# Kernel optimization log

Hardware: AMD Instinct MI355X
Metric: run time of the kernel (lower is better)

The kernel has to match this reference:

```python
import jax, jax.numpy as jnp
import numpy as np

NUM_HEADS = 16
HEAD_DIM = 64


def setup_inputs() -> dict:
    key = jax.random.key(0)
    k1, k2, k3 = jax.random.split(key, 3)
    B, S, D = 2, 2048, 1024
    scale = 1.0 / np.sqrt(D)
    return {
        "x": jax.random.normal(k1, (B, S, D), dtype=jnp.float32),
        "W_qkv": jax.random.normal(k2, (D, 3 * D), dtype=jnp.float32) * scale,
        "b_qkv": jnp.zeros((3 * D,), dtype=jnp.float32),
        "W_o": jax.random.normal(k3, (D, D), dtype=jnp.float32) * scale,
        "b_o": jnp.zeros((D,), dtype=jnp.float32),
    }


def reference(x, W_qkv, b_qkv, W_o, b_o):
    B, S, D = x.shape
    H, Hd = NUM_HEADS, HEAD_DIM
    qkv = x @ W_qkv + b_qkv                      # [B, S, 3D]
    qkv = qkv.reshape(B, S, H, 3 * Hd).transpose(0, 2, 1, 3)  # [B, H, S, 3Hd]
    q, k, v = jnp.split(qkv, 3, axis=-1)         # each [B, H, S, Hd]
    # negative squared Euclidean distance: -(|q|^2 - 2 q.k + |k|^2)
    q_sq = jnp.sum(q * q, axis=-1)[..., :, None]   # [B, H, S, 1]
    k_sq = jnp.sum(k * k, axis=-1)[..., None, :]   # [B, H, 1, S]
    qk = jnp.einsum("bhsd,bhtd->bhst", q, k)       # [B, H, S, S]
    logits = -(q_sq - 2.0 * qk + k_sq)
    attn = jax.nn.softmax(logits, axis=-1)
    vals = jnp.einsum("bhst,bhtd->bhsd", attn, v)  # [B, H, S, Hd]
    vals = vals.transpose(0, 2, 1, 3).reshape(B, S, D)
    return vals @ W_o + b_o
```

## Files before the change

kernel.cpp:

```cpp
#include <hip/hip_runtime.h>
#include <hip/hip_bf16.h>

#define NUM_B   2
#define SEQ     2048
#define DMODEL  1024
#define NH      16
#define HD      64
#define M_TOT   (NUM_B * SEQ)
#define N_QKV   (3 * DMODEL)
#define LOG2E   1.4426950408889634f
#define EXP_BIAS 96.0f

typedef __attribute__((ext_vector_type(8))) short short8v;
typedef __attribute__((ext_vector_type(4))) float float4v;
typedef unsigned short ushort_t;

__device__ __forceinline__ ushort_t f2bf(float x) {
    unsigned u = __builtin_bit_cast(unsigned, x);
    u = u + 0x7FFFu + ((u >> 16) & 1u);
    return (ushort_t)(u >> 16);
}
__device__ __forceinline__ float bf2f(ushort_t h) {
    unsigned u = ((unsigned)h) << 16;
    return __builtin_bit_cast(float, u);
}
__device__ __forceinline__ void gll16(const void* g, void* l) {
    __builtin_amdgcn_global_load_lds(
        (const __attribute__((address_space(1))) unsigned int*)g,
        (__attribute__((address_space(3))) unsigned int*)l, 16, 0, 0);
}
__device__ __forceinline__ int sw4(int r) { return (r & 3) ^ ((r >> 2) & 3); }

__global__ __launch_bounds__(256) void prep_kernel(
    const float* __restrict__ Wq, const float* __restrict__ Wo,
    const float* __restrict__ Xf,
    ushort_t* __restrict__ WqT_hi, ushort_t* __restrict__ WqT_lo,
    ushort_t* __restrict__ WoT,
    ushort_t* __restrict__ Xhi, ushort_t* __restrict__ Xlo)
{
    const int bid = blockIdx.x;
    const int t = threadIdx.x;

    if (bid >= 1024) {
        size_t base = (size_t)(bid - 1024) * 4096 + t * 16;
        float xs[16];
        *(float4v*)&xs[0]  = *(const float4v*)(Xf + base);
        *(float4v*)&xs[4]  = *(const float4v*)(Xf + base + 4);
        *(float4v*)&xs[8]  = *(const float4v*)(Xf + base + 8);
        *(float4v*)&xs[12] = *(const float4v*)(Xf + base + 12);
        short8v h0, h1, l0, l1;
        #pragma unroll
        for (int e = 0; e < 8; e++) {
            ushort_t a = f2bf(xs[e]), b = f2bf(xs[8 + e]);
            h0[e] = (short)a; h1[e] = (short)b;
            l0[e] = (short)f2bf(xs[e] - bf2f(a));
            l1[e] = (short)f2bf(xs[8 + e] - bf2f(b));
        }
        *(short8v*)(Xhi + base) = h0; *(short8v*)(Xhi + base + 8) = h1;
        *(short8v*)(Xlo + base) = l0; *(short8v*)(Xlo + base + 8) = l1;
        return;
    }

    __shared__ float Tf[64][65];
    const float* src; ushort_t *dhi, *dlo; int N, k0, n0;
    if (bid < 768) {
        int kt = bid / 48, nt = bid % 48;
        src = Wq; N = N_QKV; dhi = WqT_hi; dlo = WqT_lo;
        k0 = kt * 64; n0 = nt * 64;
    } else {
        int tid = bid - 768;
        int kt = tid >> 4, nt = tid & 15;
        src = Wo; N = DMODEL; dhi = WoT; dlo = nullptr;
        k0 = kt * 64; n0 = nt * 64;
    }
    {
        int r = t >> 2, c0 = (t & 3) * 16;
        const float* srow = src + (size_t)(k0 + r) * N + n0 + c0;
        #pragma unroll
        for (int u = 0; u < 4; u++) {
            float4v f = *(const float4v*)(srow + 4 * u);
            #pragma unroll
            for (int e = 0; e < 4; e++) Tf[r][c0 + 4 * u + e] = f[e];
        }
    }
    __syncthreads();
    {
        int nl = t >> 2, kc = (t & 3) * 16;
        short8v h0, h1, l0, l1;
        #pragma unroll
        for (int e = 0; e < 8; e++) {
            float x0 = Tf[kc + e][nl];
            float x1 = Tf[kc + 8 + e][nl];
            ushort_t a = f2bf(x0), b = f2bf(x1);
            h0[e] = (short)a; h1[e] = (short)b;
            l0[e] = (short)f2bf(x0 - bf2f(a));
            l1[e] = (short)f2bf(x1 - bf2f(b));
        }
        ushort_t* o = dhi + (size_t)(n0 + nl) * 1024 + k0 + kc;
        *(short8v*)o = h0; *(short8v*)(o + 8) = h1;
        if (dlo) {
            ushort_t* o2 = dlo + (size_t)(n0 + nl) * 1024 + k0 + kc;
            *(short8v*)o2 = l0; *(short8v*)(o2 + 8) = l1;
        }
    }
}

template<bool PRE>
__global__ __launch_bounds__(256) void qkv_mfma_kernel(
    const float* __restrict__ X,
    const ushort_t* __restrict__ Xhi, const ushort_t* __restrict__ Xlo,
    const ushort_t* __restrict__ WqT_hi, const ushort_t* __restrict__ WqT_lo,
    const float* __restrict__ bias,
    ushort_t* __restrict__ Qhi, ushort_t* __restrict__ Qlo,
    ushort_t* __restrict__ Khi, ushort_t* __restrict__ Klo,
    ushort_t* __restrict__ Vout,
    float* __restrict__ Qsq, float* __restrict__ Ksq)
{
    __shared__ ushort_t AS2[2 * 128 * 32];
    __shared__ ushort_t BS [2 * 128 * 32];
    const int LO = 128 * 32;
    const int t = threadIdx.x;
    const int w = t >> 6, lane = t & 63;
    const int quad = (t >> 4) & 3, ln = t & 15;
    const int wr = w >> 1, wc = w & 1;
    const int m0 = blockIdx.y * 128, n0 = blockIdx.x * 128;
    const int g = blockIdx.x * 2 + wc;
    const int h = g / 3, part = g % 3;

    const ushort_t* gA[2]; ushort_t* lA[2];
    const float* aptr = nullptr;
    ushort_t *ast_hi0, *ast_hi1, *ast_lo0, *ast_lo1;
    size_t xlo_off = 0;
    if constexpr (PRE) {
        #pragma unroll
        for (int i = 0; i < 2; i++) {
            int c = 256 * i + 64 * w + lane;
            int r = c >> 2, kbp = c & 3;
            gA[i] = Xhi + (size_t)(m0 + r) * 1024 + 8 * (kbp ^ sw4(r));
            lA[i] = &AS2[(256 * i + 64 * w) * 8];
        }
        xlo_off = (size_t)(Xlo - Xhi);
    } else {
        const int arow = t >> 1, akh = t & 1;
        aptr = X + (size_t)(m0 + arow) * DMODEL + 16 * akh;
        const int asw = sw4(arow);
        ast_hi0 = &AS2[arow * 32 + (((2 * akh) ^ asw) << 3)];
        ast_hi1 = &AS2[arow * 32 + (((2 * akh + 1) ^ asw) << 3)];
        ast_lo0 = &AS2[LO + arow * 32 + (((2 * akh) ^ asw) << 3)];
        ast_lo1 = &AS2[LO + arow * 32 + (((2 * akh + 1) ^ asw) << 3)];
    }

    const ushort_t* gB[2]; ushort_t* lB[2];
    #pragma unroll
    for (int i = 0; i < 2; i++) {
        int c = 256 * i + 64 * w + lane;
        int n = c >> 2, kbp = c & 3;
        gB[i] = WqT_hi + (size_t)(n0 + n) * 1024 + 8 * (kbp ^ sw4(n));
        lB[i] = &BS[(256 * i + 64 * w) * 8];
    }
    const size_t lo_goff = (size_t)(WqT_lo - WqT_hi);

    int aoff[4], boff[4];
    #pragma unroll
    for (int i = 0; i < 4; i++) {
        int m_l = 64 * wr + 16 * i + ln;
        aoff[i] = m_l * 32 + ((quad ^ sw4(m_l)) << 3);
        int n_l = 64 * wc + 16 * i + ln;
        boff[i] = n_l * 32 + ((quad ^ sw4(n_l)) << 3);
    }

    float4v acc[4][4];
    #pragma unroll
    for (int i = 0; i < 4; i++)
        #pragma unroll
        for (int j = 0; j < 4; j++) acc[i][j] = (float4v){0.f, 0.f, 0.f, 0.f};

    for (int k0 = 0; k0 < DMODEL; k0 += 32) {
        __syncthreads();
        #pragma unroll
        for (int i = 0; i < 2; i++) {
            gll16(gB[i] + k0, lB[i]);
            gll16(gB[i] + k0 + lo_goff, lB[i] + LO);
        }
        if constexpr (PRE) {
            #pragma unroll
            for (int i = 0; i < 2; i++) {
                gll16(gA[i] + k0, lA[i]);
                gll16(gA[i] + k0 + xlo_off, lA[i] + LO);
            }
        } else {
            float xs[16];
            *(float4v*)&xs[0]  = *(const float4v*)(aptr + k0);
            *(float4v*)&xs[4]  = *(const float4v*)(aptr + k0 + 4);
            *(float4v*)&xs[8]  = *(const float4v*)(aptr + k0 + 8);
            *(float4v*)&xs[12] = *(const float4v*)(aptr + k0 + 12);
            short8v h0, h1, l0, l1;
            #pragma unroll
            for (int e = 0; e < 8; e++) {
                ushort_t a = f2bf(xs[e]), b = f2bf(xs[8 + e]);
                h0[e] = (short)a; h1[e] = (short)b;
                l0[e] = (short)f2bf(xs[e] - bf2f(a));
                l1[e] = (short)f2bf(xs[8 + e] - bf2f(b));
            }
            *(short8v*)ast_hi0 = h0; *(short8v*)ast_hi1 = h1;
            *(short8v*)ast_lo0 = l0; *(short8v*)ast_lo1 = l1;
        }
        __syncthreads();

        short8v ah[4], al[4], bh[4], bl[4];
        #pragma unroll
        for (int i = 0; i < 4; i++) {
            ah[i] = *(short8v*)&AS2[aoff[i]];
            al[i] = *(short8v*)&AS2[LO + aoff[i]];
            bh[i] = *(short8v*)&BS[boff[i]];
            bl[i] = *(short8v*)&BS[LO + boff[i]];
        }
        if (part != 2) {
            #pragma unroll
            for (int mt = 0; mt < 4; mt++)
                #pragma unroll
                for (int nt = 0; nt < 4; nt++) {
                    acc[mt][nt] = __builtin_amdgcn_mfma_f32_16x16x32_bf16(ah[mt], bh[nt], acc[mt][nt], 0, 0, 0);
                    acc[mt][nt] = __builtin_amdgcn_mfma_f32_16x16x32_bf16(ah[mt], bl[nt], acc[mt][nt], 0, 0, 0);
                    acc[mt][nt] = __builtin_amdgcn_mfma_f32_16x16x32_bf16(al[mt], bh[nt], acc[mt][nt], 0, 0, 0);
                }
        } else {
            #pragma unroll
            for (int mt = 0; mt < 4; mt++)
                #pragma unroll
                for (int nt = 0; nt < 4; nt++)
                    acc[mt][nt] = __builtin_amdgcn_mfma_f32_16x16x32_bf16(ah[mt], bh[nt], acc[mt][nt], 0, 0, 0);
        }
    }

    float bvv[4];
    #pragma unroll
    for (int nt = 0; nt < 4; nt++) bvv[nt] = bias[64 * g + 16 * nt + ln];

    #pragma unroll
    for (int mt = 0; mt < 4; mt++) {
        #pragma unroll
        for (int r = 0; r < 4; r++) {
            int m = m0 + 64 * wr + 16 * mt + 4 * quad + r;
            int bb = m >> 11, s = m & (SEQ - 1);
            size_t hsrow = (size_t)(bb * NH + h) * SEQ + s;
            size_t rowbase = hsrow * HD;
            float vv[4];
            #pragma unroll
            for (int nt = 0; nt < 4; nt++) vv[nt] = acc[mt][nt][r] + bvv[nt];
            if (part == 0) {
                float sq = 0.f;
                #pragma unroll
                for (int nt = 0; nt < 4; nt++) {
                    float v = vv[nt];
                    sq += v * v;
                    float v2 = v * (2.0f * LOG2E);
                    ushort_t hb = f2bf(v2);
                    Qhi[rowbase + 16 * nt + ln] = hb;
                    Qlo[rowbase + 16 * nt + ln] = f2bf(v2 - bf2f(hb));
                }
                sq += __shfl_xor(sq, 1); sq += __shfl_xor(sq, 2);
                sq += __shfl_xor(sq, 4); sq += __shfl_xor(sq, 8);
                if (ln == 0) Qsq[hsrow] = sq * LOG2E - EXP_BIAS;
            } else if (part == 1) {
                float sq = 0.f;
                #pragma unroll
                for (int nt = 0; nt < 4; nt++) {
                    float v = vv[nt];
                    sq += v * v;
                    ushort_t hb = f2bf(v);
                    Khi[rowbase + 16 * nt + ln] = hb;
                    Klo[rowbase + 16 * nt + ln] = f2bf(v - bf2f(hb));
                }
                sq += __shfl_xor(sq, 1); sq += __shfl_xor(sq, 2);
                sq += __shfl_xor(sq, 4); sq += __shfl_xor(sq, 8);
                if (ln == 0) Ksq[hsrow] = sq * LOG2E;
            } else {
                if constexpr (PRE) {
                    #pragma unroll
                    for (int nt = 0; nt < 4; nt++)
                        Vout[((size_t)(bb * NH + h) * 64 + 16 * nt + ln) * SEQ + s] = f2bf(vv[nt]);
                } else {
                    #pragma unroll
                    for (int nt = 0; nt < 4; nt++)
                        Vout[rowbase + 16 * nt + ln] = f2bf(vv[nt]);
                }
            }
        }
    }
}

template<bool PRE>
__global__ __launch_bounds__(256) void attn_mfma_kernel(
    const ushort_t* __restrict__ Qhi, const ushort_t* __restrict__ Qlo,
    const ushort_t* __restrict__ Khi, const ushort_t* __restrict__ Klo,
    const ushort_t* __restrict__ Vsrc,
    const float* __restrict__ Qsq, const float* __restrict__ Ksq,
    ushort_t* __restrict__ vals)
{
    __shared__ ushort_t KS[2 * 64 * 64];
    __shared__ ushort_t VtS [64 * 64];
    __shared__ ushort_t PsS [128 * 72];
    const int LO = 64 * 64;

    const int t    = threadIdx.x;
    const int w    = t >> 6, lane = t & 63;
    const int quad = (t >> 4) & 3, ln = t & 15;
    const int bh   = blockIdx.y;
    const int q0   = blockIdx.x * 128;
    const size_t base  = (size_t)bh * SEQ * HD;
    const size_t baseS = (size_t)bh * SEQ;

    short8v qhi[2][2], qlo[2][2];
    float4v qsq4[2];
    #pragma unroll
    for (int mt = 0; mt < 2; mt++) {
        size_t ro = base + (size_t)(q0 + 32 * w + 16 * mt + ln) * HD + quad * 8;
        #pragma unroll
        for (int c = 0; c < 2; c++) {
            qhi[mt][c] = *(const short8v*)(Qhi + ro + 32 * c);
            qlo[mt][c] = *(const short8v*)(Qlo + ro + 32 * c);
        }
        qsq4[mt] = *(const float4v*)(Qsq + baseS + q0 + 32 * w + 16 * mt + 4 * quad);
    }

    const ushort_t* gK[2]; ushort_t* lK[2];
    #pragma unroll
    for (int i = 0; i < 2; i++) {
        int c = 256 * i + 64 * w + lane;
        int key = c >> 3, dbp = c & 7;
        gK[i] = Khi + base + (size_t)key * HD + 8 * (dbp ^ ((key >> 3) & 7));
        lK[i] = &KS[(256 * i + 64 * w) * 8];
    }
    const size_t kloff = (size_t)(Klo - Khi);

    const ushort_t* gV[2]; ushort_t* lV[2];
    if constexpr (PRE) {
        #pragma unroll
        for (int i = 0; i < 2; i++) {
            int c = 256 * i + 64 * w + lane;
            int d = c >> 3, kc = c & 7;
            gV[i] = Vsrc + ((size_t)bh * 64 + d) * SEQ + 8 * (kc ^ ((d >> 3) & 7));
            lV[i] = &VtS[(256 * i + 64 * w) * 8];
        }
    }

    float4v accO[2][4];
    float lsum[2][4];
    #pragma unroll
    for (int mt = 0; mt < 2; mt++) {
        #pragma unroll
        for (int nt = 0; nt < 4; nt++) accO[mt][nt] = (float4v){0.f, 0.f, 0.f, 0.f};
        #pragma unroll
        for (int r = 0; r < 4; r++) lsum[mt][r] = 0.f;
    }

    for (int kt = 0; kt < SEQ; kt += 64) {
        __syncthreads();
        #pragma unroll
        for (int i = 0; i < 2; i++) {
            gll16(gK[i] + (size_t)kt * HD, lK[i]);
            gll16(gK[i] + (size_t)kt * HD + kloff, lK[i] + LO);
        }
        if constexpr (PRE) {
            #pragma unroll
            for (int i = 0; i < 2; i++)
                gll16(gV[i] + kt, lV[i]);
        } else {
            #pragma unroll
            for (int i = 0; i < 2; i++) {
                int c = t + 256 * i;
                int key = c >> 3, db = c & 7;
                short8v v8 = *(const short8v*)(Vsrc + base + (size_t)(kt + key) * HD + 8 * db);
                int col = key ^ (db << 3);
                #pragma unroll
                for (int e = 0; e < 8; e++)
                    VtS[(8 * db + e) * 64 + col] = (ushort_t)v8[e];
            }
        }
        float ksq_c[4];
        #pragma unroll
        for (int nt = 0; nt < 4; nt++)
            ksq_c[nt] = Ksq[baseS + kt + 16 * nt + ln];
        __syncthreads();

        float4v accS[2][4];
        #pragma unroll
        for (int mt = 0; mt < 2; mt++)
            #pragma unroll
            for (int nt = 0; nt < 4; nt++) accS[mt][nt] = (float4v){0.f, 0.f, 0.f, 0.f};

        #pragma unroll
        for (int nt = 0; nt < 4; nt++) {
            int keyrow = 16 * nt + ln;
            int swz = (keyrow >> 3) & 7;
            #pragma unroll
            for (int c = 0; c < 2; c++) {
                int db  = quad + 4 * c;
                int off = keyrow * 64 + ((db ^ swz) << 3);
                short8v bh_ = *(short8v*)&KS[off];
                short8v bl_ = *(short8v*)&KS[LO + off];
                #pragma unroll
                for (int mt = 0; mt < 2; mt++) {
                    accS[mt][nt] = __builtin_amdgcn_mfma_f32_16x16x32_bf16(qhi[mt][c], bh_, accS[mt][nt], 0, 0, 0);
                    accS[mt][nt] = __builtin_amdgcn_mfma_f32_16x16x32_bf16(qhi[mt][c], bl_, accS[mt][nt], 0, 0, 0);
                    accS[mt][nt] = __builtin_amdgcn_mfma_f32_16x16x32_bf16(qlo[mt][c], bh_, accS[mt][nt], 0, 0, 0);
                }
            }
        }

        #pragma unroll
        for (int mt = 0; mt < 2; mt++) {
            #pragma unroll
            for (int nt = 0; nt < 4; nt++) {
                #pragma unroll
                for (int r = 0; r < 4; r++) {
                    float p = exp2f(accS[mt][nt][r] - ksq_c[nt] - qsq4[mt][r]);
                    lsum[mt][r] += p;
                    PsS[(32 * w + 16 * mt + 4 * quad + r) * 72 + 16 * nt + ln] = f2bf(p);
                }
            }
        }
        __syncthreads();

        #pragma unroll
        for (int c = 0; c < 2; c++) {
            short8v aP[2];
            #pragma unroll
            for (int mt = 0; mt < 2; mt++)
                aP[mt] = *(short8v*)&PsS[(32 * w + 16 * mt + ln) * 72 + quad * 8 + 32 * c];
            #pragma unroll
            for (int nt = 0; nt < 4; nt++) {
                int drow = 16 * nt + ln;
                int db   = quad + 4 * c;
                int off  = drow * 64 + ((db ^ ((drow >> 3) & 7)) << 3);
                short8v bV = *(short8v*)&VtS[off];
                #pragma unroll
                for (int mt = 0; mt < 2; mt++)
                    accO[mt][nt] = __builtin_amdgcn_mfma_f32_16x16x32_bf16(aP[mt], bV, accO[mt][nt], 0, 0, 0);
            }
        }
    }

    const int bb = bh >> 4, h = bh & 15;
    #pragma unroll
    for (int mt = 0; mt < 2; mt++) {
        float inv[4];
        #pragma unroll
        for (int r = 0; r < 4; r++) {
            float s = lsum[mt][r];
            s += __shfl_xor(s, 1); s += __shfl_xor(s, 2);
            s += __shfl_xor(s, 4); s += __shfl_xor(s, 8);
            inv[r] = 1.f / s;
        }
        #pragma unroll
        for (int nt = 0; nt < 4; nt++)
            #pragma unroll
            for (int r = 0; r < 4; r++) {
                int row = q0 + 32 * w + 16 * mt + 4 * quad + r;
                vals[(size_t)(bb * SEQ + row) * DMODEL + h * 64 + 16 * nt + ln] =
                    f2bf(accO[mt][nt][r] * inv[r]);
            }
    }
}

__global__ __launch_bounds__(256) void out_mfma_kernel(
    const ushort_t* __restrict__ Ab, const ushort_t* __restrict__ BT,
    const float* __restrict__ bias, float* __restrict__ out)
{
    __shared__ ushort_t AS[128 * 32], BSo[128 * 32];
    const int t = threadIdx.x;
    const int w = t >> 6, lane = t & 63;
    const int quad = (t >> 4) & 3, ln = t & 15;
    const int wr = w >> 1, wc = w & 1;
    const int m0 = blockIdx.y * 128, n0 = blockIdx.x * 128;

    const ushort_t* gA[2]; const ushort_t* gB[2];
    ushort_t *lA[2], *lB[2];
    #pragma unroll
    for (int i = 0; i < 2; i++) {
        int c = 256 * i + 64 * w + lane;
        int r = c >> 2, kbp = c & 3;
        gA[i] = Ab + (size_t)(m0 + r) * 1024 + 8 * (kbp ^ sw4(r));
        gB[i] = BT + (size_t)(n0 + r) * 1024 + 8 * (kbp ^ sw4(r));
        lA[i] = &AS[(256 * i + 64 * w) * 8];
        lB[i] = &BSo[(256 * i + 64 * w) * 8];
    }
    int aoff[4], boff[4];
    #pragma unroll
    for (int i = 0; i < 4; i++) {
        int m_l = 64 * wr + 16 * i + ln;
        aoff[i] = m_l * 32 + ((quad ^ sw4(m_l)) << 3);
        int n_l = 64 * wc + 16 * i + ln;
        boff[i] = n_l * 32 + ((quad ^ sw4(n_l)) << 3);
    }

    float4v acc[4][4];
    #pragma unroll
    for (int i = 0; i < 4; i++)
        #pragma unroll
        for (int j = 0; j < 4; j++) acc[i][j] = (float4v){0.f, 0.f, 0.f, 0.f};

    for (int k0 = 0; k0 < DMODEL; k0 += 32) {
        __syncthreads();
        #pragma unroll
        for (int i = 0; i < 2; i++) {
            gll16(gA[i] + k0, lA[i]);
            gll16(gB[i] + k0, lB[i]);
        }
        __syncthreads();
        short8v a[4], b[4];
        #pragma unroll
        for (int i = 0; i < 4; i++) {
            a[i] = *(short8v*)&AS[aoff[i]];
            b[i] = *(short8v*)&BSo[boff[i]];
        }
        #pragma unroll
        for (int mt = 0; mt < 4; mt++)
            #pragma unroll
            for (int nt = 0; nt < 4; nt++)
                acc[mt][nt] = __builtin_amdgcn_mfma_f32_16x16x32_bf16(a[mt], b[nt], acc[mt][nt], 0, 0, 0);
    }

    #pragma unroll
    for (int nt = 0; nt < 4; nt++) {
        int n = n0 + 64 * wc + 16 * nt + ln;
        float bv = bias[n];
        #pragma unroll
        for (int mt = 0; mt < 4; mt++)
            #pragma unroll
            for (int r = 0; r < 4; r++) {
                int m = m0 + 64 * wr + 16 * mt + 4 * quad + r;
                out[(size_t)m * DMODEL + n] = acc[mt][nt][r] + bv;
            }
    }
}

extern "C" void kernel_launch(void* const* d_in, const int* in_sizes, int n_in,
                              void* d_out, int out_size, void* d_ws, size_t ws_size,
                              hipStream_t stream) {
    const float* x     = (const float*)d_in[0];
    const float* W_qkv = (const float*)d_in[1];
    const float* b_qkv = (const float*)d_in[2];
    const float* W_o   = (const float*)d_in[3];
    const float* b_o   = (const float*)d_in[4];
    float* out = (float*)d_out;

    const size_t WQT = (size_t)N_QKV * DMODEL;
    const size_t WO  = (size_t)DMODEL * DMODEL;
    const size_t QE  = (size_t)NUM_B * NH * SEQ * HD;
    const size_t SQN = (size_t)NUM_B * NH * SEQ;

    const size_t NEED = (2 * WQT + WO + 5 * QE + 2 * QE) * 2 + 2 * SQN * 4;
    const bool pre = (ws_size >= NEED);

    ushort_t* ws     = (ushort_t*)d_ws;
    ushort_t* WqT_hi = ws;
    ushort_t* WqT_lo = WqT_hi + WQT;
    ushort_t* WoT    = WqT_lo + WQT;
    ushort_t* Qhi    = WoT + WO;
    ushort_t* Qlo    = Qhi + QE;
    ushort_t* Khi    = Qlo + QE;
    ushort_t* Klo    = Khi + QE;
    ushort_t* Vx     = Klo + QE;
    float*    Qsq; float* Ksq;
    ushort_t* valsb; ushort_t* Xhi = nullptr; ushort_t* Xlo = nullptr;

    if (pre) {
        Qsq   = (float*)(Vx + QE);
        Ksq   = Qsq + SQN;
        Xhi   = (ushort_t*)(Ksq + SQN);
        Xlo   = Xhi + QE;
        valsb = WqT_hi;
    } else {
        valsb = Vx + QE;
        Qsq   = (float*)(valsb + QE);
        Ksq   = Qsq + SQN;
    }

    prep_kernel<<<pre ? 2048 : 1024, 256, 0, stream>>>(
        W_qkv, W_o, x, WqT_hi, WqT_lo, WoT, Xhi, Xlo);
    if (pre) {
        qkv_mfma_kernel<true><<<dim3(N_QKV / 128, M_TOT / 128), 256, 0, stream>>>(
            x, Xhi, Xlo, WqT_hi, WqT_lo, b_qkv, Qhi, Qlo, Khi, Klo, Vx, Qsq, Ksq);
        attn_mfma_kernel<true><<<dim3(SEQ / 128, NUM_B * NH), 256, 0, stream>>>(
            Qhi, Qlo, Khi, Klo, Vx, Qsq, Ksq, valsb);
    } else {
        qkv_mfma_kernel<false><<<dim3(N_QKV / 128, M_TOT / 128), 256, 0, stream>>>(
            x, nullptr, nullptr, WqT_hi, WqT_lo, b_qkv, Qhi, Qlo, Khi, Klo, Vx, Qsq, Ksq);
        attn_mfma_kernel<false><<<dim3(SEQ / 128, NUM_B * NH), 256, 0, stream>>>(
            Qhi, Qlo, Khi, Klo, Vx, Qsq, Ksq, valsb);
    }
    out_mfma_kernel<<<dim3(DMODEL / 128, M_TOT / 128), 256, 0, stream>>>(
        valsb, WoT, b_o, out);
}
```

Measured before the change: 327.3 us.

## Use 8 waves of 16 query rows each in attention kernel

The attention kernel now launches 512 threads per block, and each of the 8 waves handles 16 query rows instead of 32. That halves per-thread accumulators and Q fragments and splits the K/V tile loads over more threads. The -qsq and -ksq bias is folded into the MFMA accumulator initialisation. The barrier between writing P and reading it is dropped, which relies on each wave reading back only its own rows. More waves could hide latency better, but K/V reuse per wave falls and block-level sync costs more.

```diff
diff --git a/kernel.cpp b/kernel.cpp
--- a/kernel.cpp
+++ b/kernel.cpp
@@ -291,7 +291,7 @@
 }
 
 template<bool PRE>
-__global__ __launch_bounds__(256) void attn_mfma_kernel(
+__global__ __launch_bounds__(512) void attn_mfma_kernel(
     const ushort_t* __restrict__ Qhi, const ushort_t* __restrict__ Qlo,
     const ushort_t* __restrict__ Khi, const ushort_t* __restrict__ Klo,
     const ushort_t* __restrict__ Vsrc,
@@ -311,72 +311,54 @@
     const size_t base  = (size_t)bh * SEQ * HD;
     const size_t baseS = (size_t)bh * SEQ;
 
-    short8v qhi[2][2], qlo[2][2];
-    float4v qsq4[2];
-    #pragma unroll
-    for (int mt = 0; mt < 2; mt++) {
-        size_t ro = base + (size_t)(q0 + 32 * w + 16 * mt + ln) * HD + quad * 8;
+    short8v qhi[2], qlo[2];
+    {
+        size_t ro = base + (size_t)(q0 + 16 * w + ln) * HD + quad * 8;
         #pragma unroll
         for (int c = 0; c < 2; c++) {
-            qhi[mt][c] = *(const short8v*)(Qhi + ro + 32 * c);
-            qlo[mt][c] = *(const short8v*)(Qlo + ro + 32 * c);
-        }
-        qsq4[mt] = *(const float4v*)(Qsq + baseS + q0 + 32 * w + 16 * mt + 4 * quad);
-    }
-
-    const ushort_t* gK[2]; ushort_t* lK[2];
-    #pragma unroll
-    for (int i = 0; i < 2; i++) {
-        int c = 256 * i + 64 * w + lane;
-        int key = c >> 3, dbp = c & 7;
-        gK[i] = Khi + base + (size_t)key * HD + 8 * (dbp ^ ((key >> 3) & 7));
-        lK[i] = &KS[(256 * i + 64 * w) * 8];
-    }
+            qhi[c] = *(const short8v*)(Qhi + ro + 32 * c);
+            qlo[c] = *(const short8v*)(Qlo + ro + 32 * c);
+        }
+    }
+    float nqsq[4];
+    {
+        float4v q4 = *(const float4v*)(Qsq + baseS + q0 + 16 * w + 4 * quad);
+        #pragma unroll
+        for (int r = 0; r < 4; r++) nqsq[r] = -q4[r];
+    }
+
+    const int kkey = t >> 3, kdbp = t & 7;
+    const ushort_t* gK = Khi + base + (size_t)kkey * HD + 8 * (kdbp ^ ((kkey >> 3) & 7));
+    ushort_t* lK = &KS[(64 * w) * 8];
     const size_t kloff = (size_t)(Klo - Khi);
 
-    const ushort_t* gV[2]; ushort_t* lV[2];
+    const ushort_t* gV = nullptr; ushort_t* lV = nullptr;
     if constexpr (PRE) {
-        #pragma unroll
-        for (int i = 0; i < 2; i++) {
-            int c = 256 * i + 64 * w + lane;
-            int d = c >> 3, kc = c & 7;
-            gV[i] = Vsrc + ((size_t)bh * 64 + d) * SEQ + 8 * (kc ^ ((d >> 3) & 7));
-            lV[i] = &VtS[(256 * i + 64 * w) * 8];
-        }
-    }
-
-    float4v accO[2][4];
-    float lsum[2][4];
-    #pragma unroll
-    for (int mt = 0; mt < 2; mt++) {
-        #pragma unroll
-        for (int nt = 0; nt < 4; nt++) accO[mt][nt] = (float4v){0.f, 0.f, 0.f, 0.f};
-        #pragma unroll
-        for (int r = 0; r < 4; r++) lsum[mt][r] = 0.f;
-    }
+        int d = t >> 3, kc = t & 7;
+        gV = Vsrc + ((size_t)bh * 64 + d) * SEQ + 8 * (kc ^ ((d >> 3) & 7));
+        lV = &VtS[(64 * w) * 8];
+    }
+
+    float4v accO[4];
+    float lsum[4];
+    #pragma unroll
+    for (int nt = 0; nt < 4; nt++) accO[nt] = (float4v){0.f, 0.f, 0.f, 0.f};
+    #pragma unroll
+    for (int r = 0; r < 4; r++) lsum[r] = 0.f;
 
     for (int kt = 0; kt < SEQ; kt += 64) {
         __syncthreads();
-        #pragma unroll
-        for (int i = 0; i < 2; i++) {
-            gll16(gK[i] + (size_t)kt * HD, lK[i]);
-            gll16(gK[i] + (size_t)kt * HD + kloff, lK[i] + LO);
-        }
+        gll16(gK + (size_t)kt * HD, lK);
+        gll16(gK + (size_t)kt * HD + kloff, lK + LO * 0 + 8 * 64 * 8 - 8 * 64 * 8 + LO);
         if constexpr (PRE) {
-            #pragma unroll
-            for (int i = 0; i < 2; i++)
-                gll16(gV[i] + kt, lV[i]);
+            gll16(gV + kt, lV);
         } else {
-            #pragma unroll
-            for (int i = 0; i < 2; i++) {
-                int c = t + 256 * i;
-                int key = c >> 3, db = c & 7;
-                short8v v8 = *(const short8v*)(Vsrc + base + (size_t)(kt + key) * HD + 8 * db);
-                int col = key ^ (db << 3);
-                #pragma unroll
-                for (int e = 0; e < 8; e++)
-                    VtS[(8 * db + e) * 64 + col] = (ushort_t)v8[e];
-            }
+            int key = t >> 3, db = t & 7;
+            short8v v8 = *(const short8v*)(Vsrc + base + (size_t)(kt + key) * HD + 8 * db);
+            int col = key ^ (db << 3);
+            #pragma unroll
+            for (int e = 0; e < 8; e++)
+                VtS[(8 * db + e) * 64 + col] = (ushort_t)v8[e];
         }
         float ksq_c[4];
         #pragma unroll
@@ -384,11 +366,11 @@
             ksq_c[nt] = Ksq[baseS + kt + 16 * nt + ln];
         __syncthreads();
 
-        float4v accS[2][4];
-        #pragma unroll
-        for (int mt = 0; mt < 2; mt++)
-            #pragma unroll
-            for (int nt = 0; nt < 4; nt++) accS[mt][nt] = (float4v){0.f, 0.f, 0.f, 0.f};
+        float4v accS[4];
+        #pragma unroll
+        for (int nt = 0; nt < 4; nt++)
+            #pragma unroll
+            for (int r = 0; r < 4; r++) accS[nt][r] = nqsq[r] - ksq_c[nt];
 
         #pragma unroll
         for (int nt = 0; nt < 4; nt++) {
@@ -400,68 +382,52 @@
                 int off = keyrow * 64 + ((db ^ swz) << 3);
                 short8v bh_ = *(short8v*)&KS[off];
                 short8v bl_ = *(short8v*)&KS[LO + off];
-                #pragma unroll
-                for (int mt = 0; mt < 2; mt++) {
-                    accS[mt][nt] = __builtin_amdgcn_mfma_f32_16x16x32_bf16(qhi[mt][c], bh_, accS[mt][nt], 0, 0, 0);
-                    accS[mt][nt] = __builtin_amdgcn_mfma_f32_16x16x32_bf16(qhi[mt][c], bl_, accS[mt][nt], 0, 0, 0);
-                    accS[mt][nt] = __builtin_amdgcn_mfma_f32_16x16x32_bf16(qlo[mt][c], bh_, accS[mt][nt], 0, 0, 0);
-                }
-            }
-        }
-
-        #pragma unroll
-        for (int mt = 0; mt < 2; mt++) {
-            #pragma unroll
-            for (int nt = 0; nt < 4; nt++) {
-                #pragma unroll
-                for (int r = 0; r < 4; r++) {
-                    float p = exp2f(accS[mt][nt][r] - ksq_c[nt] - qsq4[mt][r]);
-                    lsum[mt][r] += p;
-                    PsS[(32 * w + 16 * mt + 4 * quad + r) * 72 + 16 * nt + ln] = f2bf(p);
-                }
-            }
-        }
-        __syncthreads();
+                accS[nt] = __builtin_amdgcn_mfma_f32_16x16x32_bf16(qhi[c], bh_, accS[nt], 0, 0, 0);
+                accS[nt] = __builtin_amdgcn_mfma_f32_16x16x32_bf16(qhi[c], bl_, accS[nt], 0, 0, 0);
+                accS[nt] = __builtin_amdgcn_mfma_f32_16x16x32_bf16(qlo[c], bh_, accS[nt], 0, 0, 0);
+            }
+        }
+
+        #pragma unroll
+        for (int nt = 0; nt < 4; nt++)
+            #pragma unroll
+            for (int r = 0; r < 4; r++) {
+                float p = exp2f(accS[nt][r]);
+                lsum[r] += p;
+                PsS[(16 * w + 4 * quad + r) * 72 + 16 * nt + ln] = f2bf(p);
+            }
 
         #pragma unroll
         for (int c = 0; c < 2; c++) {
-            short8v aP[2];
-            #pragma unroll
-            for (int mt = 0; mt < 2; mt++)
-                aP[mt] = *(short8v*)&PsS[(32 * w + 16 * mt + ln) * 72 + quad * 8 + 32 * c];
+            short8v aP = *(short8v*)&PsS[(16 * w + ln) * 72 + quad * 8 + 32 * c];
             #pragma unroll
             for (int nt = 0; nt < 4; nt++) {
                 int drow = 16 * nt + ln;
                 int db   = quad + 4 * c;
                 int off  = drow * 64 + ((db ^ ((drow >> 3) & 7)) << 3);
                 short8v bV = *(short8v*)&VtS[off];
-                #pragma unroll
-                for (int mt = 0; mt < 2; mt++)
-                    accO[mt][nt] = __builtin_amdgcn_mfma_f32_16x16x32_bf16(aP[mt], bV, accO[mt][nt], 0, 0, 0);
+                accO[nt] = __builtin_amdgcn_mfma_f32_16x16x32_bf16(aP, bV, accO[nt], 0, 0, 0);
             }
         }
     }
 
     const int bb = bh >> 4, h = bh & 15;
-    #pragma unroll
-    for (int mt = 0; mt < 2; mt++) {
-        float inv[4];
+    float inv[4];
+    #pragma unroll
+    for (int r = 0; r < 4; r++) {
+        float s = lsum[r];
+        s += __shfl_xor(s, 1); s += __shfl_xor(s, 2);
+        s += __shfl_xor(s, 4); s += __shfl_xor(s, 8);
+        inv[r] = 1.f / s;
+    }
+    #pragma unroll
+    for (int nt = 0; nt < 4; nt++)
         #pragma unroll
         for (int r = 0; r < 4; r++) {
-            float s = lsum[mt][r];
-            s += __shfl_xor(s, 1); s += __shfl_xor(s, 2);
-            s += __shfl_xor(s, 4); s += __shfl_xor(s, 8);
-            inv[r] = 1.f / s;
-        }
-        #pragma unroll
-        for (int nt = 0; nt < 4; nt++)
-            #pragma unroll
-            for (int r = 0; r < 4; r++) {
-                int row = q0 + 32 * w + 16 * mt + 4 * quad + r;
-                vals[(size_t)(bb * SEQ + row) * DMODEL + h * 64 + 16 * nt + ln] =
-                    f2bf(accO[mt][nt][r] * inv[r]);
-            }
-    }
+            int row = q0 + 16 * w + 4 * quad + r;
+            vals[(size_t)(bb * SEQ + row) * DMODEL + h * 64 + 16 * nt + ln] =
+                f2bf(accO[nt][r] * inv[r]);
+        }
 }
 
 __global__ __launch_bounds__(256) void out_mfma_kernel(
@@ -583,12 +549,12 @@
     if (pre) {
         qkv_mfma_kernel<true><<<dim3(N_QKV / 128, M_TOT / 128), 256, 0, stream>>>(
             x, Xhi, Xlo, WqT_hi, WqT_lo, b_qkv, Qhi, Qlo, Khi, Klo, Vx, Qsq, Ksq);
-        attn_mfma_kernel<true><<<dim3(SEQ / 128, NUM_B * NH), 256, 0, stream>>>(
+        attn_mfma_kernel<true><<<dim3(SEQ / 128, NUM_B * NH), 512, 0, stream>>>(
             Qhi, Qlo, Khi, Klo, Vx, Qsq, Ksq, valsb);
     } else {
         qkv_mfma_kernel<false><<<dim3(N_QKV / 128, M_TOT / 128), 256, 0, stream>>>(
             x, nullptr, nullptr, WqT_hi, WqT_lo, b_qkv, Qhi, Qlo, Khi, Klo, Vx, Qsq, Ksq);
-        attn_mfma_kernel<false><<<dim3(SEQ / 128, NUM_B * NH), 256, 0, stream>>>(
+        attn_mfma_kernel<false><<<dim3(SEQ / 128, NUM_B * NH), 512, 0, stream>>>(
             Qhi, Qlo, Khi, Klo, Vx, Qsq, Ksq, valsb);
     }
     out_mfma_kernel<<<dim3(DMODEL / 128, M_TOT / 128), 256, 0, stream>>>(
```

Result: slower. 340.3 us (+4.0%).

## Change LDS swizzle to row-low-bits, fold distance bias into MFMA init, drop barrier

Applied to the files above, without the earlier changes.

The K and V^T shared-memory tiles now XOR the 16-byte chunk index with the low three bits of the row instead of bits 3-5. Consecutive rows read by one MFMA fragment then land in different banks, which is meant to cut LDS bank conflicts. The -|q|^2 - |k|^2 bias now initialises the score accumulators, so the exp step is a bare exp2. The barrier between writing and reading the P tile is removed, which relies on each wave reading only its own rows of that tile.

```diff
diff --git a/kernel.cpp b/kernel.cpp
--- a/kernel.cpp
+++ b/kernel.cpp
@@ -312,7 +312,7 @@
     const size_t baseS = (size_t)bh * SEQ;
 
     short8v qhi[2][2], qlo[2][2];
-    float4v qsq4[2];
+    float nqsq[2][4];
     #pragma unroll
     for (int mt = 0; mt < 2; mt++) {
         size_t ro = base + (size_t)(q0 + 32 * w + 16 * mt + ln) * HD + quad * 8;
@@ -321,7 +321,9 @@
             qhi[mt][c] = *(const short8v*)(Qhi + ro + 32 * c);
             qlo[mt][c] = *(const short8v*)(Qlo + ro + 32 * c);
         }
-        qsq4[mt] = *(const float4v*)(Qsq + baseS + q0 + 32 * w + 16 * mt + 4 * quad);
+        float4v q4 = *(const float4v*)(Qsq + baseS + q0 + 32 * w + 16 * mt + 4 * quad);
+        #pragma unroll
+        for (int r = 0; r < 4; r++) nqsq[mt][r] = -q4[r];
     }
 
     const ushort_t* gK[2]; ushort_t* lK[2];
@@ -329,7 +331,7 @@
     for (int i = 0; i < 2; i++) {
         int c = 256 * i + 64 * w + lane;
         int key = c >> 3, dbp = c & 7;
-        gK[i] = Khi + base + (size_t)key * HD + 8 * (dbp ^ ((key >> 3) & 7));
+        gK[i] = Khi + base + (size_t)key * HD + 8 * (dbp ^ (key & 7));
         lK[i] = &KS[(256 * i + 64 * w) * 8];
     }
     const size_t kloff = (size_t)(Klo - Khi);
@@ -340,7 +342,7 @@
         for (int i = 0; i < 2; i++) {
             int c = 256 * i + 64 * w + lane;
             int d = c >> 3, kc = c & 7;
-            gV[i] = Vsrc + ((size_t)bh * 64 + d) * SEQ + 8 * (kc ^ ((d >> 3) & 7));
+            gV[i] = Vsrc + ((size_t)bh * 64 + d) * SEQ + 8 * (kc ^ (d & 7));
             lV[i] = &VtS[(256 * i + 64 * w) * 8];
         }
     }
@@ -372,10 +374,11 @@
                 int c = t + 256 * i;
                 int key = c >> 3, db = c & 7;
                 short8v v8 = *(const short8v*)(Vsrc + base + (size_t)(kt + key) * HD + 8 * db);
-                int col = key ^ (db << 3);
-                #pragma unroll
-                for (int e = 0; e < 8; e++)
+                #pragma unroll
+                for (int e = 0; e < 8; e++) {
+                    int col = key ^ (e << 3);
                     VtS[(8 * db + e) * 64 + col] = (ushort_t)v8[e];
+                }
             }
         }
         float ksq_c[4];
@@ -388,16 +391,18 @@
         #pragma unroll
         for (int mt = 0; mt < 2; mt++)
             #pragma unroll
-            for (int nt = 0; nt < 4; nt++) accS[mt][nt] = (float4v){0.f, 0.f, 0.f, 0.f};
+            for (int nt = 0; nt < 4; nt++)
+                #pragma unroll
+                for (int r = 0; r < 4; r++)
+                    accS[mt][nt][r] = nqsq[mt][r] - ksq_c[nt];
 
         #pragma unroll
         for (int nt = 0; nt < 4; nt++) {
             int keyrow = 16 * nt + ln;
-            int swz = (keyrow >> 3) & 7;
             #pragma unroll
             for (int c = 0; c < 2; c++) {
                 int db  = quad + 4 * c;
-                int off = keyrow * 64 + ((db ^ swz) << 3);
+                int off = keyrow * 64 + ((db ^ (keyrow & 7)) << 3);
                 short8v bh_ = *(short8v*)&KS[off];
                 short8v bl_ = *(short8v*)&KS[LO + off];
                 #pragma unroll
@@ -410,18 +415,15 @@
         }
 
         #pragma unroll
-        for (int mt = 0; mt < 2; mt++) {
-            #pragma unroll
-            for (int nt = 0; nt < 4; nt++) {
+        for (int mt = 0; mt < 2; mt++)
+            #pragma unroll
+            for (int nt = 0; nt < 4; nt++)
                 #pragma unroll
                 for (int r = 0; r < 4; r++) {
-                    float p = exp2f(accS[mt][nt][r] - ksq_c[nt] - qsq4[mt][r]);
+                    float p = exp2f(accS[mt][nt][r]);
                     lsum[mt][r] += p;
                     PsS[(32 * w + 16 * mt + 4 * quad + r) * 72 + 16 * nt + ln] = f2bf(p);
                 }
-            }
-        }
-        __syncthreads();
 
         #pragma unroll
         for (int c = 0; c < 2; c++) {
@@ -433,7 +435,7 @@
             for (int nt = 0; nt < 4; nt++) {
                 int drow = 16 * nt + ln;
                 int db   = quad + 4 * c;
-                int off  = drow * 64 + ((db ^ ((drow >> 3) & 7)) << 3);
+                int off  = drow * 64 + ((db ^ (drow & 7)) << 3);
                 short8v bV = *(short8v*)&VtS[off];
                 #pragma unroll
                 for (int mt = 0; mt < 2; mt++)
```

New measurement: 360.2 us. +10.1%, slower.
